# Performance work log

Measured on AMD Instinct MI355X. Metric: run time of the kernel, lower is better.

## Reference

```python
import jax, jax.numpy as jnp
import numpy as np

N = 6144
IN_DIM = 128
HEAD_DIM = 32
NUM_HEADS = 4
HIDDEN = HEAD_DIM * NUM_HEADS  # 128
EMBED = 128


def setup_inputs() -> dict:
    key = jax.random.key(0)
    ks = jax.random.split(key, 6)
    x = jax.random.normal(ks[0], (N, IN_DIM), dtype=jnp.float32)
    # per-head GAT params (stacked over heads)
    W = jax.random.normal(ks[1], (NUM_HEADS, IN_DIM, HEAD_DIM), dtype=jnp.float32) * (1.0 / np.sqrt(IN_DIM))
    a_src = jax.random.normal(ks[2], (NUM_HEADS, HEAD_DIM), dtype=jnp.float32) * (1.0 / np.sqrt(HEAD_DIM))
    a_dst = jax.random.normal(ks[3], (NUM_HEADS, HEAD_DIM), dtype=jnp.float32) * (1.0 / np.sqrt(HEAD_DIM))
    # final linear fc2: hidden -> embed (stored as (hidden, embed) so y = h @ W_fc + b_fc)
    W_fc = jax.random.normal(ks[4], (HIDDEN, EMBED), dtype=jnp.float32) * (1.0 / np.sqrt(HIDDEN))
    b_fc = jax.random.normal(ks[5], (EMBED,), dtype=jnp.float32) * 0.01
    return {"x": x, "W": W, "a_src": a_src, "a_dst": a_dst, "W_fc": W_fc, "b_fc": b_fc}


def reference(x, W, a_src, a_dst, W_fc, b_fc):
    # Wh: (H, N, D)
    Wh = jnp.einsum('nf,hfd->hnd', x, W)
    e_s = jnp.einsum('hnd,hd->hn', Wh, a_src)  # (H, N)
    e_d = jnp.einsum('hnd,hd->hn', Wh, a_dst)  # (H, N)
    # full-graph additive scores: e[h,i,j] = e_s[h,i] + e_d[h,j]
    e = e_s[:, :, None] + e_d[:, None, :]      # (H, N, N)
    att = jax.nn.softmax(jax.nn.leaky_relu(e, negative_slope=0.01), axis=-1)
    hp = jax.nn.elu(jnp.einsum('hnm,hmd->hnd', att, Wh))  # (H, N, D)
    # concat heads along feature dim -> (N, H*D)
    h = jnp.transpose(hp, (1, 0, 2)).reshape(x.shape[0], -1)
    h = jax.nn.relu(h)
    h_mean = jnp.mean(h, axis=0)               # (HIDDEN,)
    return h_mean @ W_fc + b_fc                # (EMBED,)
```

## Files before the change

kernel.cpp:

```cpp
#include <hip/hip_runtime.h>
#include <stdint.h>

#define N      6144
#define F      128
#define D      32
#define H      4
#define HID    128
#define BINS   4096
#define RLO    (-6.0f)
#define INVW   (BINS / 12.0f)
#define NC     68
#define NROWS  (BINS + 1)

__device__ __align__(16) float g_wht[(size_t)H * D * N];
__device__ float g_es[H * N];
__device__ float g_e1[H * N];
__device__ float g_e2[H * N];
__device__ int   g_bin[H * N];
__device__ __align__(16) float g_pref[(size_t)H * NROWS * NC];
__device__ float g_PART[96 * 32];

__global__ __launch_bounds__(256) void k1_gemm(const float* __restrict__ x,
                                               const float* __restrict__ W,
                                               const float* __restrict__ a_src,
                                               const float* __restrict__ a_dst) {
    int tid  = threadIdx.x;
    int wv   = tid >> 6;
    int lane = tid & 63;
    int rg   = wv & 1;
    int ch   = wv >> 1;
    int row0 = __builtin_amdgcn_readfirstlane(blockIdx.x * 8 + rg * 4);
    int col  = ch * 64 + lane;
    int h    = col >> 5;
    int d    = col & 31;
    const float* __restrict__ xr = x + (size_t)row0 * F;
    const float* __restrict__ Wp = W + h * (F * D) + d;
    float acc[4] = {0.f, 0.f, 0.f, 0.f};
#pragma unroll 4
    for (int f = 0; f < F; ++f) {
        float w = Wp[f * D];
        acc[0] = fmaf(xr[f],         w, acc[0]);
        acc[1] = fmaf(xr[F + f],     w, acc[1]);
        acc[2] = fmaf(xr[2 * F + f], w, acc[2]);
        acc[3] = fmaf(xr[3 * F + f], w, acc[3]);
    }
    float as = a_src[col], ad = a_dst[col];
#pragma unroll
    for (int r = 0; r < 4; ++r) {
        int n = row0 + r;
        float ts = acc[r] * as, td = acc[r] * ad;
#pragma unroll
        for (int m = 1; m < 32; m <<= 1) {
            ts += __shfl_xor(ts, m);
            td += __shfl_xor(td, m);
        }
        if ((lane & 31) == 0) {
            g_es[h * N + n] = ts;
            float e1 = expf(0.01f * td);
            float e2 = expf(td);
            g_e1[h * N + n] = e1;
            g_e2[h * N + n] = e2;
            int b = (int)floorf((td - RLO) * INVW);
            g_bin[h * N + n] = min(max(b, 0), BINS - 1);
        }
    }
    float4 w4;
    w4.x = acc[0]; w4.y = acc[1]; w4.z = acc[2]; w4.w = acc[3];
    *(float4*)&g_wht[(size_t)(h * 32 + d) * N + row0] = w4;
}

__global__ __launch_bounds__(256) void k2_bin_scan() {
    __shared__ float bins[BINS];
    __shared__ float tsum[256];
    int bidx = blockIdx.x;
    int h = bidx / 66, c = bidx % 66;
    int tid = threadIdx.x;
    for (int i = tid; i < BINS; i += 256) bins[i] = 0.f;
    __syncthreads();

    const int*   bi = g_bin + h * N;
    const float* ev = (((c < 32) || (c == 64)) ? g_e1 : g_e2) + h * N;
    if (c < 64) {
        const float* wcol = g_wht + (size_t)(h * 32 + (c & 31)) * N;
        for (int n = tid; n < N; n += 256)
            atomicAdd(&bins[bi[n]], ev[n] * wcol[n]);
    } else {
        for (int n = tid; n < N; n += 256)
            atomicAdd(&bins[bi[n]], ev[n]);
    }
    __syncthreads();

    int t0 = tid * 16;
    float incl[16];
    float run = 0.f;
#pragma unroll
    for (int j = 0; j < 16; ++j) { run += bins[t0 + j]; incl[j] = run; }
    tsum[tid] = run;
    for (int off = 1; off < 256; off <<= 1) {
        __syncthreads();
        float t = (tid >= off) ? tsum[tid - off] : 0.f;
        __syncthreads();
        tsum[tid] += t;
    }
    float offset = tsum[tid] - run;
    float* dst = g_pref + (size_t)h * NROWS * NC + c;
    if (tid == 0) dst[0] = 0.f;
#pragma unroll
    for (int j = 0; j < 16; ++j)
        dst[(size_t)(t0 + j + 1) * NC] = offset + incl[j];
}

__global__ __launch_bounds__(256) void k3_eval() {
    __shared__ float tot[NC];
    __shared__ float wred[4][32];
    int bidx = blockIdx.x;
    int h = bidx / 24;
    int tid = threadIdx.x;
    int lane = tid & 63, wv = tid >> 6;
    const float* hp = g_pref + (size_t)h * NROWS * NC;
    if (tid < NC) tot[tid] = hp[(size_t)BINS * NC + tid];
    __syncthreads();

    int i = (bidx % 24) * 256 + tid;
    float s = g_es[h * N + i];
    float th = -s;
    int idx = (int)floorf((th - RLO) * INVW);
    int row = min(max(idx + 1, 0), BINS);
    const float4* rp4 = (const float4*)(hp + (size_t)row * NC);
    float e1 = expf(0.01f * s), e2 = expf(s);
    float4 sc = rp4[16];
    float denom = e1 * sc.x + e2 * (tot[65] - sc.y);
    float inv = 1.0f / denom;

    float av[32];
#pragma unroll
    for (int g = 0; g < 8; ++g) {
        float4 u4 = rp4[g];
        float4 v4 = rp4[8 + g];
        float us[4] = {u4.x, u4.y, u4.z, u4.w};
        float vs[4] = {v4.x, v4.y, v4.z, v4.w};
#pragma unroll
        for (int k = 0; k < 4; ++k) {
            int dd = g * 4 + k;
            float num = e1 * us[k] + e2 * (tot[32 + dd] - vs[k]);
            av[dd] = fmaxf(num, 0.f) * inv;
        }
    }
#pragma unroll
    for (int dd = 0; dd < 32; ++dd) {
#pragma unroll
        for (int m = 1; m < 64; m <<= 1) av[dd] += __shfl_xor(av[dd], m);
    }
    if (lane == 0) {
#pragma unroll
        for (int dd = 0; dd < 32; ++dd) wred[wv][dd] = av[dd];
    }
    __syncthreads();
    if (tid < 32)
        g_PART[bidx * 32 + tid] =
            wred[0][tid] + wred[1][tid] + wred[2][tid] + wred[3][tid];
}

__global__ __launch_bounds__(128) void k4_out(const float* __restrict__ W_fc,
                                              const float* __restrict__ b_fc,
                                              float* __restrict__ out) {
    __shared__ float hm[128];
    int tid = threadIdx.x;
    {
        int hh = tid >> 5, dd = tid & 31;
        float sum = 0.f;
        for (int ch = 0; ch < 24; ++ch)
            sum += g_PART[((hh * 24 + ch) * 32) + dd];
        hm[tid] = sum * (1.0f / (float)N);
    }
    __syncthreads();
    float y = b_fc[tid];
#pragma unroll 8
    for (int c = 0; c < 128; ++c)
        y = fmaf(hm[c], W_fc[c * 128 + tid], y);
    out[tid] = y;
}

extern "C" void kernel_launch(void* const* d_in, const int* in_sizes, int n_in,
                              void* d_out, int out_size, void* d_ws, size_t ws_size,
                              hipStream_t stream) {
    (void)in_sizes; (void)n_in; (void)d_ws; (void)ws_size; (void)out_size;
    const float* x     = (const float*)d_in[0];
    const float* W     = (const float*)d_in[1];
    const float* a_src = (const float*)d_in[2];
    const float* a_dst = (const float*)d_in[3];
    const float* W_fc  = (const float*)d_in[4];
    const float* b_fc  = (const float*)d_in[5];
    float* out = (float*)d_out;

    k1_gemm<<<dim3(N / 8), dim3(256), 0, stream>>>(x, W, a_src, a_dst);
    k2_bin_scan<<<dim3(H * 66), dim3(256), 0, stream>>>();
    k3_eval<<<dim3(96), dim3(256), 0, stream>>>();
    k4_out<<<dim3(1), dim3(128), 0, stream>>>(W_fc, b_fc, out);
}
```

Before: 57.41 us.

## Fuse paired prefix columns per block and fold final linear into eval kernel

k1 now stores only the raw destination score, and k2 computes the bin index and both exponentials on the fly. Each k2 block builds the U and V prefix columns for one (head, dim) together, so the bin computation and the weight-column read are shared and the grid halves to 132 blocks of 512 threads. The prefix row stride is padded to 80 floats. k3 uses 48 larger blocks, and the last block to finish, found with an atomic counter, does the mean and the fc2 matvec, which removes the separate k4 launch. The risks are atomic-contention on shared memory with two bins per element, fewer blocks per kernel, and the correctness of the counter-reset protocol.

```diff
diff --git a/kernel.cpp b/kernel.cpp
--- a/kernel.cpp
+++ b/kernel.cpp
@@ -9,16 +9,15 @@
 #define BINS   4096
 #define RLO    (-6.0f)
 #define INVW   (BINS / 12.0f)
-#define NC     68
+#define NCP    80
 #define NROWS  (BINS + 1)
 
 __device__ __align__(16) float g_wht[(size_t)H * D * N];
 __device__ float g_es[H * N];
-__device__ float g_e1[H * N];
-__device__ float g_e2[H * N];
-__device__ int   g_bin[H * N];
-__device__ __align__(16) float g_pref[(size_t)H * NROWS * NC];
-__device__ float g_PART[96 * 32];
+__device__ float g_td[H * N];
+__device__ __align__(16) float g_pref[(size_t)H * NROWS * NCP];
+__device__ float g_PART[48 * 32];
+__device__ unsigned g_done;
 
 __global__ __launch_bounds__(256) void k1_gemm(const float* __restrict__ x,
                                                const float* __restrict__ W,
@@ -56,12 +55,7 @@
         }
         if ((lane & 31) == 0) {
             g_es[h * N + n] = ts;
-            float e1 = expf(0.01f * td);
-            float e2 = expf(td);
-            g_e1[h * N + n] = e1;
-            g_e2[h * N + n] = e2;
-            int b = (int)floorf((td - RLO) * INVW);
-            g_bin[h * N + n] = min(max(b, 0), BINS - 1);
+            g_td[h * N + n] = td;
         }
     }
     float4 w4;
@@ -69,64 +63,95 @@
     *(float4*)&g_wht[(size_t)(h * 32 + d) * N + row0] = w4;
 }
 
-__global__ __launch_bounds__(256) void k2_bin_scan() {
-    __shared__ float bins[BINS];
-    __shared__ float tsum[256];
+__global__ __launch_bounds__(512) void k2_bin_scan() {
+    __shared__ float binU[BINS];
+    __shared__ float binV[BINS];
+    __shared__ float tsum[512];
     int bidx = blockIdx.x;
-    int h = bidx / 66, c = bidx % 66;
     int tid = threadIdx.x;
-    for (int i = tid; i < BINS; i += 256) bins[i] = 0.f;
-    __syncthreads();
-
-    const int*   bi = g_bin + h * N;
-    const float* ev = (((c < 32) || (c == 64)) ? g_e1 : g_e2) + h * N;
-    if (c < 64) {
-        const float* wcol = g_wht + (size_t)(h * 32 + (c & 31)) * N;
-        for (int n = tid; n < N; n += 256)
-            atomicAdd(&bins[bi[n]], ev[n] * wcol[n]);
+    int h, cU, cV;
+    const float* wcol = nullptr;
+    if (bidx < 128) {
+        h = bidx >> 5;
+        int d = bidx & 31;
+        cU = d; cV = 32 + d;
+        wcol = g_wht + (size_t)(h * 32 + d) * N;
     } else {
-        for (int n = tid; n < N; n += 256)
-            atomicAdd(&bins[bi[n]], ev[n]);
-    }
-    __syncthreads();
-
-    int t0 = tid * 16;
-    float incl[16];
-    float run = 0.f;
-#pragma unroll
-    for (int j = 0; j < 16; ++j) { run += bins[t0 + j]; incl[j] = run; }
-    tsum[tid] = run;
-    for (int off = 1; off < 256; off <<= 1) {
+        h = bidx - 128;
+        cU = 64; cV = 65;
+    }
+    for (int i = tid; i < BINS; i += 512) { binU[i] = 0.f; binV[i] = 0.f; }
+    __syncthreads();
+
+    const float* tdp = g_td + h * N;
+    if (wcol) {
+        for (int n = tid; n < N; n += 512) {
+            float t = tdp[n];
+            float w = wcol[n];
+            int b = (int)floorf((t - RLO) * INVW);
+            b = min(max(b, 0), BINS - 1);
+            atomicAdd(&binU[b], expf(0.01f * t) * w);
+            atomicAdd(&binV[b], expf(t) * w);
+        }
+    } else {
+        for (int n = tid; n < N; n += 512) {
+            float t = tdp[n];
+            int b = (int)floorf((t - RLO) * INVW);
+            b = min(max(b, 0), BINS - 1);
+            atomicAdd(&binU[b], expf(0.01f * t));
+            atomicAdd(&binV[b], expf(t));
+        }
+    }
+    __syncthreads();
+
+    float* hp = g_pref + (size_t)h * NROWS * NCP;
+#pragma unroll
+    for (int pass = 0; pass < 2; ++pass) {
+        const float* bins = pass ? binV : binU;
+        int c = pass ? cV : cU;
+        int t0 = tid * 8;
+        float incl[8];
+        float run = 0.f;
+#pragma unroll
+        for (int j = 0; j < 8; ++j) { run += bins[t0 + j]; incl[j] = run; }
+        tsum[tid] = run;
+        for (int off = 1; off < 512; off <<= 1) {
+            __syncthreads();
+            float t = (tid >= off) ? tsum[tid - off] : 0.f;
+            __syncthreads();
+            tsum[tid] += t;
+        }
+        float offset = tsum[tid] - run;
+        float* dst = hp + c;
+        if (tid == 0) dst[0] = 0.f;
+#pragma unroll
+        for (int j = 0; j < 8; ++j)
+            dst[(size_t)(t0 + j + 1) * NCP] = offset + incl[j];
         __syncthreads();
-        float t = (tid >= off) ? tsum[tid - off] : 0.f;
-        __syncthreads();
-        tsum[tid] += t;
-    }
-    float offset = tsum[tid] - run;
-    float* dst = g_pref + (size_t)h * NROWS * NC + c;
-    if (tid == 0) dst[0] = 0.f;
-#pragma unroll
-    for (int j = 0; j < 16; ++j)
-        dst[(size_t)(t0 + j + 1) * NC] = offset + incl[j];
-}
-
-__global__ __launch_bounds__(256) void k3_eval() {
-    __shared__ float tot[NC];
-    __shared__ float wred[4][32];
+    }
+}
+
+__global__ __launch_bounds__(512) void k3_eval(const float* __restrict__ W_fc,
+                                               const float* __restrict__ b_fc,
+                                               float* __restrict__ out) {
+    __shared__ float tot[68];
+    __shared__ float wred[8][32];
+    __shared__ float hm[HID];
+    __shared__ unsigned s_rank;
     int bidx = blockIdx.x;
-    int h = bidx / 24;
+    int h = bidx / 12;
     int tid = threadIdx.x;
     int lane = tid & 63, wv = tid >> 6;
-    const float* hp = g_pref + (size_t)h * NROWS * NC;
-    if (tid < NC) tot[tid] = hp[(size_t)BINS * NC + tid];
-    __syncthreads();
-
-    int i = (bidx % 24) * 256 + tid;
+    const float* hp = g_pref + (size_t)h * NROWS * NCP;
+    if (tid < 68) tot[tid] = hp[(size_t)BINS * NCP + tid];
+    __syncthreads();
+
+    int i = (bidx % 12) * 512 + tid;
     float s = g_es[h * N + i];
     float th = -s;
     int idx = (int)floorf((th - RLO) * INVW);
     int row = min(max(idx + 1, 0), BINS);
-    const float4* rp4 = (const float4*)(hp + (size_t)row * NC);
+    const float4* rp4 = (const float4*)(hp + (size_t)row * NCP);
     float e1 = expf(0.01f * s), e2 = expf(s);
     float4 sc = rp4[16];
     float denom = e1 * sc.x + e2 * (tot[65] - sc.y);
@@ -156,29 +181,41 @@
         for (int dd = 0; dd < 32; ++dd) wred[wv][dd] = av[dd];
     }
     __syncthreads();
-    if (tid < 32)
-        g_PART[bidx * 32 + tid] =
-            wred[0][tid] + wred[1][tid] + wred[2][tid] + wred[3][tid];
-}
-
-__global__ __launch_bounds__(128) void k4_out(const float* __restrict__ W_fc,
-                                              const float* __restrict__ b_fc,
-                                              float* __restrict__ out) {
-    __shared__ float hm[128];
-    int tid = threadIdx.x;
-    {
-        int hh = tid >> 5, dd = tid & 31;
-        float sum = 0.f;
-        for (int ch = 0; ch < 24; ++ch)
-            sum += g_PART[((hh * 24 + ch) * 32) + dd];
-        hm[tid] = sum * (1.0f / (float)N);
-    }
-    __syncthreads();
-    float y = b_fc[tid];
+    if (tid < 32) {
+        float p = 0.f;
+#pragma unroll
+        for (int ww = 0; ww < 8; ++ww) p += wred[ww][tid];
+        g_PART[bidx * 32 + tid] = p;
+    }
+    __syncthreads();
+    if (tid == 0) {
+        __builtin_amdgcn_fence(__ATOMIC_RELEASE, "agent");
+        s_rank = __hip_atomic_fetch_add(&g_done, 1u,
+                     __ATOMIC_ACQ_REL, __HIP_MEMORY_SCOPE_AGENT);
+    }
+    __syncthreads();
+    if (s_rank == 47u) {
+        __builtin_amdgcn_fence(__ATOMIC_ACQUIRE, "agent");
+        if (tid < HID) {
+            int hh = tid >> 5, dd = tid & 31;
+            float sum = 0.f;
+#pragma unroll
+            for (int ch = 0; ch < 12; ++ch)
+                sum += g_PART[((hh * 12 + ch) * 32) + dd];
+            hm[tid] = sum * (1.0f / (float)N);
+        }
+        __syncthreads();
+        if (tid < 128) {
+            float y = b_fc[tid];
 #pragma unroll 8
-    for (int c = 0; c < 128; ++c)
-        y = fmaf(hm[c], W_fc[c * 128 + tid], y);
-    out[tid] = y;
+            for (int c = 0; c < 128; ++c)
+                y = fmaf(hm[c], W_fc[c * 128 + tid], y);
+            out[tid] = y;
+        }
+        if (tid == 0)
+            __hip_atomic_store(&g_done, 0u,
+                               __ATOMIC_RELAXED, __HIP_MEMORY_SCOPE_AGENT);
+    }
 }
 
 extern "C" void kernel_launch(void* const* d_in, const int* in_sizes, int n_in,
@@ -194,7 +231,6 @@
     float* out = (float*)d_out;
 
     k1_gemm<<<dim3(N / 8), dim3(256), 0, stream>>>(x, W, a_src, a_dst);
-    k2_bin_scan<<<dim3(H * 66), dim3(256), 0, stream>>>();
-    k3_eval<<<dim3(96), dim3(256), 0, stream>>>();
-    k4_out<<<dim3(1), dim3(128), 0, stream>>>(W_fc, b_fc, out);
-}
+    k2_bin_scan<<<dim3(132), dim3(512), 0, stream>>>();
+    k3_eval<<<dim3(48), dim3(512), 0, stream>>>(W_fc, b_fc, out);
+}
```

After: 64.82 us. +12.9%, slower.
